# Kernel optimization log

Measured on AMD Instinct MI355X. Metric: run time of the kernel, lower is better.

## Reference

```python
import math
import jax, jax.numpy as jnp
import numpy as np

B, N, D = 16, 2048, 64

def setup_inputs() -> dict:
    key = jax.random.key(0)
    kq, kk, kv, kl = jax.random.split(key, 4)
    q = jax.random.normal(kq, (B, N, D), dtype=jnp.float32)
    k = jax.random.normal(kk, (B, N, D), dtype=jnp.float32)
    v = jax.random.normal(kv, (B, N, D), dtype=jnp.float32)
    valid = jax.random.randint(kl, (B, N), 0, 2048, dtype=jnp.int64 if jax.config.jax_enable_x64 else jnp.int32)
    return {"q": q, "k": k, "v": v, "valid": valid}

def reference(q, k, v, valid):
    # scores[b,i,j] = <q[b,i], k[b,j]> / sqrt(d)
    d = k.shape[-1]
    scores = jnp.einsum('bid,bjd->bij', q, k) / jnp.sqrt(jnp.asarray(d, q.dtype))
    # mask[b,i,j] = (j+1) > valid[b,i]; masked positions replaced by 1e-6
    # (faithful to torch.masked_fill(scores, mask, 1e-06) -- NOT -inf)
    key_pos = jnp.arange(1, scores.shape[-1] + 1)  # [N]
    mask = key_pos[None, None, :] > valid[:, :, None]  # [B,N,N]
    mask_scores = jnp.where(mask, jnp.asarray(1e-06, scores.dtype), scores)
    weights = jax.nn.softmax(mask_scores, axis=-1)
    # dropout p=0.0 -> identity
    return jnp.einsum('bij,bjd->bid', weights, v)
```

## Files before the change

kernel.cpp:

```cpp
#include <hip/hip_runtime.h>
#include <hip/hip_bf16.h>
#include <stdint.h>

#define BB 16
#define NN 2048
#define DD 64
#define BM 64
#define BN 64
#define KSTR 72
#define PSTR 72

typedef __attribute__((ext_vector_type(8))) short short8;
typedef __attribute__((ext_vector_type(4))) float f32x4;

__device__ __forceinline__ unsigned short f2bf(float f) {
  union { float f; uint32_t u; } c; c.f = f;
  uint32_t u = c.u + 0x7fffu + ((c.u >> 16) & 1u);
  return (unsigned short)(u >> 16);
}
__device__ __forceinline__ uint32_t pkrn(float a, float b) {
  union { __hip_bfloat162 h; uint32_t u; } c;
  c.h = __float22bfloat162_rn(make_float2(a, b));
  return c.u;
}

#define QSCALE 0.18033688f
#define CMW 1.0000010f

__global__ __launch_bounds__(256) void prep_kernel(const float* __restrict__ k,
                                                   const float* __restrict__ v,
                                                   const int* __restrict__ valid,
                                                   unsigned short* __restrict__ kbf,
                                                   unsigned short* __restrict__ vt,
                                                   int* __restrict__ perm,
                                                   int* __restrict__ sval,
                                                   float* __restrict__ suf) {
  __shared__ float t[64][65];
  __shared__ int hist[2048];
  __shared__ int part[256];
  __shared__ float ts[32][16];
  int id = blockIdx.x, tid = threadIdx.x;
  if (id < 512) {
#pragma unroll
    for (int r = 0; r < 4; r++) {
      int i = (id * 4 + r) * 256 + tid;
      float4 f = ((const float4*)k)[i];
      ushort4 o;
      o.x = f2bf(f.x); o.y = f2bf(f.y); o.z = f2bf(f.z); o.w = f2bf(f.w);
      ((ushort4*)kbf)[i] = o;
    }
  } else if (id < 1024) {
    int bid = id - 512;
    int b = bid >> 5;
    int k0 = (bid & 31) * 64;
    const float4* src = (const float4*)(v + ((size_t)b * NN + k0) * DD);
#pragma unroll
    for (int i = 0; i < 4; i++) {
      int f4 = tid + i * 256;
      int row = f4 >> 4, c4 = f4 & 15;
      float4 f = src[f4];
      t[row][c4*4+0] = f.x; t[row][c4*4+1] = f.y; t[row][c4*4+2] = f.z; t[row][c4*4+3] = f.w;
    }
    __syncthreads();
    int d = tid >> 2, kg = tid & 3;
    unsigned short* dst = vt + ((size_t)b * DD + d) * NN + k0 + kg * 16;
#pragma unroll
    for (int u = 0; u < 4; u++) {
      ushort4 o;
      o.x = f2bf(t[kg*16+u*4+0][d]);
      o.y = f2bf(t[kg*16+u*4+1][d]);
      o.z = f2bf(t[kg*16+u*4+2][d]);
      o.w = f2bf(t[kg*16+u*4+3][d]);
      ((ushort4*)dst)[u] = o;
    }
  } else if (id < 1040) {
    int b = id - 1024;
    for (int i = tid; i < 2048; i += 256) hist[i] = 0;
    __syncthreads();
    for (int i = tid; i < NN; i += 256) atomicAdd(&hist[valid[b * NN + i]], 1);
    __syncthreads();
    int base = tid * 8, loc[8], s = 0;
#pragma unroll
    for (int j = 0; j < 8; j++) { loc[j] = s; s += hist[base + j]; }
    part[tid] = s;
    __syncthreads();
    if (tid == 0) {
      int run = 0;
      for (int t2 = 0; t2 < 256; t2++) { int tmp = part[t2]; part[t2] = run; run += tmp; }
    }
    __syncthreads();
#pragma unroll
    for (int j = 0; j < 8; j++) hist[base + j] = part[tid] + loc[j];
    __syncthreads();
    for (int i = tid; i < NN; i += 256) {
      int vv = valid[b * NN + i];
      int pos = atomicAdd(&hist[vv], 1);
      perm[b * NN + pos] = i;
      sval[b * NN + pos] = vv;
    }
  } else {
    int sb = id - 1040;
    int b = sb >> 2, dg = sb & 3;
    for (int p = tid; p < 512; p += 256) {
      int tt = p >> 4, d0 = p & 15;
      const float* vp = v + ((size_t)b * NN + tt * 64) * DD + dg * 16 + d0;
      float s = 0.0f;
#pragma unroll 8
      for (int r = 0; r < 64; r++) s += vp[(size_t)r * DD];
      ts[tt][d0] = s;
    }
    __syncthreads();
    if (tid < 16) {
      int d = dg * 16 + tid;
      float acc = 0.0f;
      suf[((size_t)b * 33 + 32) * 64 + d] = 0.0f;
      for (int tt = 31; tt >= 0; tt--) {
        acc += ts[tt][tid];
        suf[((size_t)b * 33 + tt) * 64 + d] = acc;
      }
    }
  }
}

template <int NS>
__global__ __launch_bounds__(256, 4) void attn_kernel(
    const float* __restrict__ q, const unsigned short* __restrict__ kbf,
    const unsigned short* __restrict__ vtbf, const int* __restrict__ perm,
    const int* __restrict__ sval, const float* __restrict__ suf,
    float* __restrict__ out, unsigned short* __restrict__ po,
    float* __restrict__ pz)
{
  constexpr int JLEN = NN / NS;

  __shared__ __align__(16) unsigned short Klds[BN * KSTR];
  __shared__ __align__(16) unsigned short Vlds[DD * KSTR];
  __shared__ __align__(16) unsigned short Plds[4 * 16 * PSTR];
  __shared__ int vld[BM];
  __shared__ int pidx[BM];

  int id = blockIdx.x;
  int b = (id & 7) + 8 * ((id >> 3) & 1);
  int rest = id >> 4;
  int sp = rest % NS;
  int qt = 31 - (rest / NS);
  int i0 = qt * BM;
  int jbase = sp * JLEN;
  int rangeEnd = jbase + JLEN;

  int tid = threadIdx.x;
  int w = tid >> 6, lane = tid & 63;
  int m = lane & 15, quad = lane >> 4;

  if (tid < BM) {
    vld[tid]  = sval[b * NN + i0 + tid];
    pidx[tid] = perm[b * NN + i0 + tid];
  }
  int maxv = sval[b * NN + i0 + 63];
  int jcov = ((maxv + 63) >> 6) << 6;
  int niter = (min(rangeEnd, jcov) - jbase) >> 6;
  if (niter < 0) niter = 0;
  int Tp = (jbase >> 6) + niter;

  __syncthreads();

  f32x4 o[4] = {{0,0,0,0},{0,0,0,0},{0,0,0,0},{0,0,0,0}};
  float z = 0.0f;

  if (niter > 0) {
    int vq = vld[w * 16 + m];
    int qrow = pidx[w * 16 + m];

    short8 qf[2];
    {
      const float* qp = q + ((size_t)b * NN + qrow) * DD;
#pragma unroll
      for (int s = 0; s < 2; s++) {
        float4 f0 = *(const float4*)(qp + s * 32 + quad * 8);
        float4 f1 = *(const float4*)(qp + s * 32 + quad * 8 + 4);
        union { short8 v; uint32_t x[4]; } tmp;
        tmp.x[0] = pkrn(f0.x * QSCALE, f0.y * QSCALE);
        tmp.x[1] = pkrn(f0.z * QSCALE, f0.w * QSCALE);
        tmp.x[2] = pkrn(f1.x * QSCALE, f1.y * QSCALE);
        tmp.x[3] = pkrn(f1.z * QSCALE, f1.w * QSCALE);
        qf[s] = tmp.v;
      }
    }

    unsigned short* pbase = Plds + w * 16 * PSTR;
    int srow = tid >> 2, scol = (tid & 3) * 16;
    const unsigned short* gk = kbf + ((size_t)(b * NN + jbase + srow)) * DD + scol;
    const unsigned short* gv = vtbf + ((size_t)b * DD + srow) * NN + jbase + scol;

    uint4 ka = *(const uint4*)gk, kb2 = *(const uint4*)(gk + 8);
    uint4 va = *(const uint4*)gv, vb2 = *(const uint4*)(gv + 8);

    for (int it = 0; it < niter; ++it) {
      int j0 = jbase + it * BN;
      __syncthreads();
      *(uint4*)&Klds[srow * KSTR + scol]     = ka;
      *(uint4*)&Klds[srow * KSTR + scol + 8] = kb2;
      *(uint4*)&Vlds[srow * KSTR + scol]     = va;
      *(uint4*)&Vlds[srow * KSTR + scol + 8] = vb2;
      if (it + 1 < niter) {
        gk += BN * DD; gv += BN;
        ka = *(const uint4*)gk; kb2 = *(const uint4*)(gk + 8);
        va = *(const uint4*)gv; vb2 = *(const uint4*)(gv + 8);
      }
      __syncthreads();

      f32x4 s[4] = {{0,0,0,0},{0,0,0,0},{0,0,0,0},{0,0,0,0}};
#pragma unroll
      for (int c = 0; c < 4; c++) {
#pragma unroll
        for (int ss = 0; ss < 2; ss++) {
          short8 kf = *(const short8*)&Klds[(c * 16 + m) * KSTR + ss * 32 + quad * 8];
          s[c] = __builtin_amdgcn_mfma_f32_16x16x32_bf16(kf, qf[ss], s[c], 0, 0, 0);
        }
      }

#pragma unroll
      for (int c = 0; c < 4; c++) {
        float e[4];
#pragma unroll
        for (int rr = 0; rr < 4; rr++) {
          int j = j0 + c * 16 + quad * 4 + rr;
          float ex = __builtin_amdgcn_exp2f(s[c][rr]);
          e[rr] = (j < vq) ? ex : CMW;
        }
        z += (e[0] + e[1]) + (e[2] + e[3]);
        *(uint2*)&pbase[m * PSTR + c * 16 + quad * 4] =
            make_uint2(pkrn(e[0], e[1]), pkrn(e[2], e[3]));
      }

      __builtin_amdgcn_s_waitcnt(0xc07f);

#pragma unroll
      for (int ss = 0; ss < 2; ss++) {
        short8 pf = *(const short8*)&pbase[m * PSTR + ss * 32 + quad * 8];
#pragma unroll
        for (int t = 0; t < 4; t++) {
          short8 vf = *(const short8*)&Vlds[(t * 16 + m) * KSTR + ss * 32 + quad * 8];
          o[t] = __builtin_amdgcn_mfma_f32_16x16x32_bf16(vf, pf, o[t], 0, 0, 0);
        }
      }
    }
  }

  z += __shfl_xor(z, 16);
  z += __shfl_xor(z, 32);
  z += CMW * (float)(rangeEnd - (Tp << 6));

  {
    const float* sh = suf + ((size_t)b * 33 + Tp) * 64;
    const float* se = suf + ((size_t)b * 33 + (rangeEnd >> 6)) * 64;
#pragma unroll
    for (int t = 0; t < 4; t++) {
      float4 a = *(const float4*)&sh[t * 16 + quad * 4];
      float4 e4 = *(const float4*)&se[t * 16 + quad * 4];
      o[t][0] += CMW * (a.x - e4.x);
      o[t][1] += CMW * (a.y - e4.y);
      o[t][2] += CMW * (a.z - e4.z);
      o[t][3] += CMW * (a.w - e4.w);
    }
  }

  if (NS > 1) {
    int rrow = i0 + w * 16 + m;
    unsigned short* op = po + ((size_t)((sp * BB + b) * NN) + rrow) * DD;
#pragma unroll
    for (int t = 0; t < 4; t++)
      *(uint2*)&op[t * 16 + quad * 4] = make_uint2(pkrn(o[t][0], o[t][1]),
                                                   pkrn(o[t][2], o[t][3]));
    if (quad == 0) pz[(size_t)(sp * BB + b) * NN + rrow] = z;
  } else {
    float inv = 1.0f / z;
    int qrow = pidx[w * 16 + m];
    float* op2 = out + ((size_t)b * NN + qrow) * DD;
#pragma unroll
    for (int t = 0; t < 4; t++)
      *(float4*)&op2[t * 16 + quad * 4] =
          make_float4(o[t][0]*inv, o[t][1]*inv, o[t][2]*inv, o[t][3]*inv);
  }
}

template <int NS>
__global__ __launch_bounds__(256) void combine_kernel(const unsigned short* __restrict__ po,
                                                      const float* __restrict__ pz,
                                                      const int* __restrict__ perm,
                                                      float* __restrict__ out) {
  int gid = blockIdx.x * 256 + threadIdx.x;
  size_t base = (size_t)gid * 8;
  int rowr = gid >> 3;
  float r[8] = {0,0,0,0,0,0,0,0};
  float zs = 0.0f;
#pragma unroll
  for (int sp = 0; sp < NS; sp++) {
    uint4 a = *(const uint4*)(po + (size_t)sp * BB * NN * DD + base);
    zs += pz[(size_t)sp * BB * NN + rowr];
    uint32_t aw[4] = {a.x, a.y, a.z, a.w};
#pragma unroll
    for (int i = 0; i < 4; i++) {
      r[2*i]   += __uint_as_float(aw[i] << 16);
      r[2*i+1] += __uint_as_float(aw[i] & 0xffff0000u);
    }
  }
  float inv = 1.0f / zs;
  int b = rowr >> 11;
  int qrow = perm[rowr];
  float* op = out + ((size_t)(b * NN + qrow)) * DD + (gid & 7) * 8;
  *(float4*)&op[0] = make_float4(r[0]*inv, r[1]*inv, r[2]*inv, r[3]*inv);
  *(float4*)&op[4] = make_float4(r[4]*inv, r[5]*inv, r[6]*inv, r[7]*inv);
}

extern "C" void kernel_launch(void* const* d_in, const int* in_sizes, int n_in,
                              void* d_out, int out_size, void* d_ws, size_t ws_size,
                              hipStream_t stream) {
  const float* q = (const float*)d_in[0];
  const float* k = (const float*)d_in[1];
  const float* v = (const float*)d_in[2];
  const int* valid = (const int*)d_in[3];
  float* out = (float*)d_out;

  unsigned short* kbf  = (unsigned short*)d_ws;
  unsigned short* vtbf = kbf + (size_t)BB * NN * DD;
  unsigned short* po   = vtbf + (size_t)BB * NN * DD;
  float* pz   = (float*)(po + (size_t)4 * BB * NN * DD);
  int*   perm = (int*)(pz + (size_t)4 * BB * NN);
  int*   sv   = perm + (size_t)BB * NN;
  float* suf  = (float*)(sv + (size_t)BB * NN);

  size_t need4 = ((char*)(suf + (size_t)BB * 33 * DD)) - (char*)d_ws;

  hipLaunchKernelGGL(prep_kernel, dim3(1104), dim3(256), 0, stream,
                     k, v, valid, kbf, vtbf, perm, sv, suf);
  if (ws_size >= need4) {
    hipLaunchKernelGGL((attn_kernel<4>), dim3(16 * 32 * 4), dim3(256), 0, stream,
                       q, kbf, vtbf, perm, sv, suf, out, po, pz);
    hipLaunchKernelGGL((combine_kernel<4>), dim3(1024), dim3(256), 0, stream,
                       po, pz, perm, out);
  } else {
    hipLaunchKernelGGL((attn_kernel<1>), dim3(16 * 32), dim3(256), 0, stream,
                       q, kbf, vtbf, perm, sv, suf, out, po, pz);
  }
}
```

Measured before the change: 114.9 us.

## Use 128-row query tiles with interleaved key-split and fused V tile sums

The attention block grows to 128 query rows across 512 threads, so each staged K/V tile in shared memory serves twice as many rows. The key split changes from contiguous quarters to interleaved 64-key tiles (sp + NS*i), which evens out work across splits for the sorted valid lengths. Each half of the block skips compute past its own coverage while still helping load tiles. Per-tile V column sums are now computed inside the V transpose blocks, which removes the separate suffix-sum blocks. Masked tails are then accumulated per tile instead of from a suffix difference. The cost is half as many attention blocks, more registers per block, and idle half-blocks on tiles past their coverage.

```diff
diff --git a/kernel.cpp b/kernel.cpp
--- a/kernel.cpp
+++ b/kernel.cpp
@@ -5,7 +5,7 @@
 #define BB 16
 #define NN 2048
 #define DD 64
-#define BM 64
+#define BM 128
 #define BN 64
 #define KSTR 72
 #define PSTR 72
@@ -34,11 +34,10 @@
                                                    unsigned short* __restrict__ vt,
                                                    int* __restrict__ perm,
                                                    int* __restrict__ sval,
-                                                   float* __restrict__ suf) {
+                                                   float* __restrict__ tsum) {
   __shared__ float t[64][65];
   __shared__ int hist[2048];
   __shared__ int part[256];
-  __shared__ float ts[32][16];
   int id = blockIdx.x, tid = threadIdx.x;
   if (id < 512) {
 #pragma unroll
@@ -73,7 +72,16 @@
       o.w = f2bf(t[kg*16+u*4+3][d]);
       ((ushort4*)dst)[u] = o;
     }
-  } else if (id < 1040) {
+    if (tid < 64) {
+      float s0 = 0.0f, s1 = 0.0f, s2 = 0.0f, s3 = 0.0f;
+#pragma unroll 4
+      for (int kk = 0; kk < 64; kk += 4) {
+        s0 += t[kk+0][tid]; s1 += t[kk+1][tid];
+        s2 += t[kk+2][tid]; s3 += t[kk+3][tid];
+      }
+      tsum[((size_t)b * 32 + (k0 >> 6)) * 64 + tid] = (s0 + s1) + (s2 + s3);
+    }
+  } else {
     int b = id - 1024;
     for (int i = tid; i < 2048; i += 256) hist[i] = 0;
     __syncthreads();
@@ -98,43 +106,22 @@
       perm[b * NN + pos] = i;
       sval[b * NN + pos] = vv;
     }
-  } else {
-    int sb = id - 1040;
-    int b = sb >> 2, dg = sb & 3;
-    for (int p = tid; p < 512; p += 256) {
-      int tt = p >> 4, d0 = p & 15;
-      const float* vp = v + ((size_t)b * NN + tt * 64) * DD + dg * 16 + d0;
-      float s = 0.0f;
-#pragma unroll 8
-      for (int r = 0; r < 64; r++) s += vp[(size_t)r * DD];
-      ts[tt][d0] = s;
-    }
-    __syncthreads();
-    if (tid < 16) {
-      int d = dg * 16 + tid;
-      float acc = 0.0f;
-      suf[((size_t)b * 33 + 32) * 64 + d] = 0.0f;
-      for (int tt = 31; tt >= 0; tt--) {
-        acc += ts[tt][tid];
-        suf[((size_t)b * 33 + tt) * 64 + d] = acc;
-      }
-    }
   }
 }
 
 template <int NS>
-__global__ __launch_bounds__(256, 4) void attn_kernel(
+__global__ __launch_bounds__(512, 4) void attn_kernel(
     const float* __restrict__ q, const unsigned short* __restrict__ kbf,
     const unsigned short* __restrict__ vtbf, const int* __restrict__ perm,
-    const int* __restrict__ sval, const float* __restrict__ suf,
+    const int* __restrict__ sval, const float* __restrict__ tsum,
     float* __restrict__ out, unsigned short* __restrict__ po,
     float* __restrict__ pz)
 {
-  constexpr int JLEN = NN / NS;
+  constexpr int NT = 32 / NS;
 
   __shared__ __align__(16) unsigned short Klds[BN * KSTR];
   __shared__ __align__(16) unsigned short Vlds[DD * KSTR];
-  __shared__ __align__(16) unsigned short Plds[4 * 16 * PSTR];
+  __shared__ __align__(16) unsigned short Plds[8 * 16 * PSTR];
   __shared__ int vld[BM];
   __shared__ int pidx[BM];
 
@@ -142,33 +129,32 @@
   int b = (id & 7) + 8 * ((id >> 3) & 1);
   int rest = id >> 4;
   int sp = rest % NS;
-  int qt = 31 - (rest / NS);
-  int i0 = qt * BM;
-  int jbase = sp * JLEN;
-  int rangeEnd = jbase + JLEN;
+  int u = 15 - rest / NS;
+  int i0 = u * BM;
 
   int tid = threadIdx.x;
   int w = tid >> 6, lane = tid & 63;
   int m = lane & 15, quad = lane >> 4;
+  int h = w >> 2, wq = w & 3;
+  int row = h * 64 + wq * 16 + m;
 
   if (tid < BM) {
     vld[tid]  = sval[b * NN + i0 + tid];
     pidx[tid] = perm[b * NN + i0 + tid];
   }
-  int maxv = sval[b * NN + i0 + 63];
-  int jcov = ((maxv + 63) >> 6) << 6;
-  int niter = (min(rangeEnd, jcov) - jbase) >> 6;
-  if (niter < 0) niter = 0;
-  int Tp = (jbase >> 6) + niter;
+  int Th = (sval[b * NN + i0 + h * 64 + 63] + 63) >> 6;
+  int T1 = (sval[b * NN + i0 + 127] + 63) >> 6;
+  int nh     = (Th - sp + NS - 1) / NS;
+  int nstage = (T1 - sp + NS - 1) / NS;
 
   __syncthreads();
 
   f32x4 o[4] = {{0,0,0,0},{0,0,0,0},{0,0,0,0},{0,0,0,0}};
   float z = 0.0f;
 
-  if (niter > 0) {
-    int vq = vld[w * 16 + m];
-    int qrow = pidx[w * 16 + m];
+  if (nstage > 0) {
+    int vq = vld[row];
+    int qrow = pidx[row];
 
     short8 qf[2];
     {
@@ -187,60 +173,59 @@
     }
 
     unsigned short* pbase = Plds + w * 16 * PSTR;
-    int srow = tid >> 2, scol = (tid & 3) * 16;
-    const unsigned short* gk = kbf + ((size_t)(b * NN + jbase + srow)) * DD + scol;
-    const unsigned short* gv = vtbf + ((size_t)b * DD + srow) * NN + jbase + scol;
-
-    uint4 ka = *(const uint4*)gk, kb2 = *(const uint4*)(gk + 8);
-    uint4 va = *(const uint4*)gv, vb2 = *(const uint4*)(gv + 8);
-
-    for (int it = 0; it < niter; ++it) {
-      int j0 = jbase + it * BN;
+    int srow = tid >> 3, scol = (tid & 7) * 8;
+    const unsigned short* gk = kbf + ((size_t)(b * NN + sp * BN + srow)) * DD + scol;
+    const unsigned short* gv = vtbf + ((size_t)b * DD + srow) * NN + sp * BN + scol;
+
+    uint4 ka = *(const uint4*)gk;
+    uint4 va = *(const uint4*)gv;
+
+    for (int it = 0; it < nstage; ++it) {
+      int j0 = (sp + NS * it) * BN;
       __syncthreads();
-      *(uint4*)&Klds[srow * KSTR + scol]     = ka;
-      *(uint4*)&Klds[srow * KSTR + scol + 8] = kb2;
-      *(uint4*)&Vlds[srow * KSTR + scol]     = va;
-      *(uint4*)&Vlds[srow * KSTR + scol + 8] = vb2;
-      if (it + 1 < niter) {
-        gk += BN * DD; gv += BN;
-        ka = *(const uint4*)gk; kb2 = *(const uint4*)(gk + 8);
-        va = *(const uint4*)gv; vb2 = *(const uint4*)(gv + 8);
+      *(uint4*)&Klds[srow * KSTR + scol] = ka;
+      *(uint4*)&Vlds[srow * KSTR + scol] = va;
+      if (it + 1 < nstage) {
+        gk += (size_t)NS * BN * DD; gv += NS * BN;
+        ka = *(const uint4*)gk; va = *(const uint4*)gv;
       }
       __syncthreads();
 
-      f32x4 s[4] = {{0,0,0,0},{0,0,0,0},{0,0,0,0},{0,0,0,0}};
-#pragma unroll
-      for (int c = 0; c < 4; c++) {
+      if (it < nh) {
+        f32x4 s[4] = {{0,0,0,0},{0,0,0,0},{0,0,0,0},{0,0,0,0}};
+#pragma unroll
+        for (int c = 0; c < 4; c++) {
+#pragma unroll
+          for (int ss = 0; ss < 2; ss++) {
+            short8 kf = *(const short8*)&Klds[(c * 16 + m) * KSTR + ss * 32 + quad * 8];
+            s[c] = __builtin_amdgcn_mfma_f32_16x16x32_bf16(kf, qf[ss], s[c], 0, 0, 0);
+          }
+        }
+
+#pragma unroll
+        for (int c = 0; c < 4; c++) {
+          float e[4];
+#pragma unroll
+          for (int rr = 0; rr < 4; rr++) {
+            int j = j0 + c * 16 + quad * 4 + rr;
+            float ex = __builtin_amdgcn_exp2f(s[c][rr]);
+            e[rr] = (j < vq) ? ex : CMW;
+          }
+          z += (e[0] + e[1]) + (e[2] + e[3]);
+          *(uint2*)&pbase[m * PSTR + c * 16 + quad * 4] =
+              make_uint2(pkrn(e[0], e[1]), pkrn(e[2], e[3]));
+        }
+
+        __builtin_amdgcn_s_waitcnt(0xc07f);
+
 #pragma unroll
         for (int ss = 0; ss < 2; ss++) {
-          short8 kf = *(const short8*)&Klds[(c * 16 + m) * KSTR + ss * 32 + quad * 8];
-          s[c] = __builtin_amdgcn_mfma_f32_16x16x32_bf16(kf, qf[ss], s[c], 0, 0, 0);
-        }
-      }
-
-#pragma unroll
-      for (int c = 0; c < 4; c++) {
-        float e[4];
-#pragma unroll
-        for (int rr = 0; rr < 4; rr++) {
-          int j = j0 + c * 16 + quad * 4 + rr;
-          float ex = __builtin_amdgcn_exp2f(s[c][rr]);
-          e[rr] = (j < vq) ? ex : CMW;
-        }
-        z += (e[0] + e[1]) + (e[2] + e[3]);
-        *(uint2*)&pbase[m * PSTR + c * 16 + quad * 4] =
-            make_uint2(pkrn(e[0], e[1]), pkrn(e[2], e[3]));
-      }
-
-      __builtin_amdgcn_s_waitcnt(0xc07f);
-
-#pragma unroll
-      for (int ss = 0; ss < 2; ss++) {
-        short8 pf = *(const short8*)&pbase[m * PSTR + ss * 32 + quad * 8];
-#pragma unroll
-        for (int t = 0; t < 4; t++) {
-          short8 vf = *(const short8*)&Vlds[(t * 16 + m) * KSTR + ss * 32 + quad * 8];
-          o[t] = __builtin_amdgcn_mfma_f32_16x16x32_bf16(vf, pf, o[t], 0, 0, 0);
+          short8 pf = *(const short8*)&pbase[m * PSTR + ss * 32 + quad * 8];
+#pragma unroll
+          for (int t = 0; t < 4; t++) {
+            short8 vf = *(const short8*)&Vlds[(t * 16 + m) * KSTR + ss * 32 + quad * 8];
+            o[t] = __builtin_amdgcn_mfma_f32_16x16x32_bf16(vf, pf, o[t], 0, 0, 0);
+          }
         }
       }
     }
@@ -248,24 +233,25 @@
 
   z += __shfl_xor(z, 16);
   z += __shfl_xor(z, 32);
-  z += CMW * (float)(rangeEnd - (Tp << 6));
+  z += CMW * (float)((NT - nh) * 64);
 
   {
-    const float* sh = suf + ((size_t)b * 33 + Tp) * 64;
-    const float* se = suf + ((size_t)b * 33 + (rangeEnd >> 6)) * 64;
-#pragma unroll
-    for (int t = 0; t < 4; t++) {
-      float4 a = *(const float4*)&sh[t * 16 + quad * 4];
-      float4 e4 = *(const float4*)&se[t * 16 + quad * 4];
-      o[t][0] += CMW * (a.x - e4.x);
-      o[t][1] += CMW * (a.y - e4.y);
-      o[t][2] += CMW * (a.z - e4.z);
-      o[t][3] += CMW * (a.w - e4.w);
+    const float* tb = tsum + (size_t)b * 32 * 64;
+    for (int i = nh; i < NT; ++i) {
+      const float* tr = tb + (sp + NS * i) * 64;
+#pragma unroll
+      for (int t = 0; t < 4; t++) {
+        float4 a = *(const float4*)&tr[t * 16 + quad * 4];
+        o[t][0] += CMW * a.x;
+        o[t][1] += CMW * a.y;
+        o[t][2] += CMW * a.z;
+        o[t][3] += CMW * a.w;
+      }
     }
   }
 
   if (NS > 1) {
-    int rrow = i0 + w * 16 + m;
+    int rrow = i0 + row;
     unsigned short* op = po + ((size_t)((sp * BB + b) * NN) + rrow) * DD;
 #pragma unroll
     for (int t = 0; t < 4; t++)
@@ -274,7 +260,7 @@
     if (quad == 0) pz[(size_t)(sp * BB + b) * NN + rrow] = z;
   } else {
     float inv = 1.0f / z;
-    int qrow = pidx[w * 16 + m];
+    int qrow = pidx[row];
     float* op2 = out + ((size_t)b * NN + qrow) * DD;
 #pragma unroll
     for (int t = 0; t < 4; t++)
@@ -327,19 +313,19 @@
   float* pz   = (float*)(po + (size_t)4 * BB * NN * DD);
   int*   perm = (int*)(pz + (size_t)4 * BB * NN);
   int*   sv   = perm + (size_t)BB * NN;
-  float* suf  = (float*)(sv + (size_t)BB * NN);
-
-  size_t need4 = ((char*)(suf + (size_t)BB * 33 * DD)) - (char*)d_ws;
-
-  hipLaunchKernelGGL(prep_kernel, dim3(1104), dim3(256), 0, stream,
-                     k, v, valid, kbf, vtbf, perm, sv, suf);
+  float* tsum = (float*)(sv + (size_t)BB * NN);
+
+  size_t need4 = ((char*)(tsum + (size_t)BB * 32 * DD)) - (char*)d_ws;
+
+  hipLaunchKernelGGL(prep_kernel, dim3(1040), dim3(256), 0, stream,
+                     k, v, valid, kbf, vtbf, perm, sv, tsum);
   if (ws_size >= need4) {
-    hipLaunchKernelGGL((attn_kernel<4>), dim3(16 * 32 * 4), dim3(256), 0, stream,
-                       q, kbf, vtbf, perm, sv, suf, out, po, pz);
+    hipLaunchKernelGGL((attn_kernel<4>), dim3(16 * 16 * 4), dim3(512), 0, stream,
+                       q, kbf, vtbf, perm, sv, tsum, out, po, pz);
     hipLaunchKernelGGL((combine_kernel<4>), dim3(1024), dim3(256), 0, stream,
                        po, pz, perm, out);
   } else {
-    hipLaunchKernelGGL((attn_kernel<1>), dim3(16 * 32), dim3(256), 0, stream,
-                       q, kbf, vtbf, perm, sv, suf, out, po, pz);
-  }
-}
+    hipLaunchKernelGGL((attn_kernel<1>), dim3(16 * 16), dim3(512), 0, stream,
+                       q, kbf, vtbf, perm, sv, tsum, out, po, pz);
+  }
+}
```

New measurement: 111.2 us. -3.2%, faster.
